# Kernel tuning notes

Measured on AMD Instinct MI355X. Metric: run time of the kernel, lower is better.

The kernel has to match this reference:

```python
import jax, jax.numpy as jnp
import numpy as np

D = 256          # hidden_dim
H = 4            # num_heads
HD = D // H      # head_dim = 64
E = 4            # num_experts (hard-coded in MoE)
TOPK = 2         # top_k (hard-coded)
DFF = 2 * D      # expert ffn width
EPS = 1e-5


def _ln(x, g, b):
    mu = x.mean(-1, keepdims=True)
    var = x.var(-1, keepdims=True)  # biased, matches torch LayerNorm
    return (x - mu) * jax.lax.rsqrt(var + EPS) * g + b


def _ff(x, w1, b1, w2, b2):
    h = jax.nn.gelu(x @ w1 + b1, approximate=False)  # torch nn.GELU default = exact erf
    return h @ w2 + b2


def setup_inputs() -> dict:
    key = jax.random.key(0)
    ks = jax.random.split(key, 24)
    B, S, IN = 4, 2048, 256
    s = 0.02
    inp = {
        'x': jax.random.normal(ks[0], (B, S, IN), jnp.float32),
        'mask': jax.random.randint(ks[1], (B, S), 0, 2).astype(jnp.int32),
        'w_in': jax.random.normal(ks[2], (IN, D), jnp.float32) * s,
        'b_in': jnp.zeros((D,), jnp.float32),
        'g1': jnp.ones((D,), jnp.float32),
        'be1': jnp.zeros((D,), jnp.float32),
        'wq': jax.random.normal(ks[3], (D, D), jnp.float32) * s,
        'bq': jnp.zeros((D,), jnp.float32),
        'wk': jax.random.normal(ks[4], (D, D), jnp.float32) * s,
        'bk': jnp.zeros((D,), jnp.float32),
        'wv': jax.random.normal(ks[5], (D, D), jnp.float32) * s,
        'bv': jnp.zeros((D,), jnp.float32),
        'wo': jax.random.normal(ks[6], (D, D), jnp.float32) * s,
        'bo': jnp.zeros((D,), jnp.float32),
        'g2': jnp.ones((D,), jnp.float32),
        'be2': jnp.zeros((D,), jnp.float32),
        'wg': jax.random.normal(ks[7], (D, E), jnp.float32) * s,
        'bg': jnp.zeros((E,), jnp.float32),
        'ew1': jax.random.normal(ks[8], (E, D, DFF), jnp.float32) * s,
        'eb1': jnp.zeros((E, DFF), jnp.float32),
        'ew2': jax.random.normal(ks[9], (E, DFF, D), jnp.float32) * s,
        'eb2': jnp.zeros((E, D), jnp.float32),
    }
    return inp


def reference(x, mask, w_in, b_in, g1, be1, wq, bq, wk, bk, wv, bv, wo, bo, g2, be2, wg, bg, ew1, eb1, ew2, eb2):
    B, S, _ = x.shape
    x = x @ w_in + b_in
    res = x
    h = _ln(x, g1, be1)
    q = (h @ wq + bq).reshape(B, S, H, HD).transpose(0, 2, 1, 3)  # bhsd
    k = (h @ wk + bk).reshape(B, S, H, HD).transpose(0, 2, 1, 3)
    v = (h @ wv + bv).reshape(B, S, H, HD).transpose(0, 2, 1, 3)
    # RoPE (interleaved pairs, half-concat output, as in source)
    inv_freq = 1.0 / (10000.0 ** (jnp.arange(0, HD, 2, dtype=jnp.float32) / HD))
    ang = jnp.arange(S, dtype=jnp.float32)[:, None] * inv_freq[None, :]  # [S, HD//2]
    sin, cos = jnp.sin(ang), jnp.cos(ang)  # broadcast over (B,H)
    def rot(t):
        ts = t.reshape(B, H, S, HD // 2, 2)
        t0, t1 = ts[..., 0], ts[..., 1]
        return jnp.concatenate([t0 * cos - t1 * sin, t1 * cos + t0 * sin], axis=-1)
    qr, kr = rot(q), rot(k)
    attn = jnp.einsum('bhqd,bhkd->bhqk', qr, kr) * (HD ** -0.5)
    row = mask[:, None, :, None]  # [B,1,S,1] -> masks whole query rows
    attn = jnp.where(row == 0, jnp.float32(-1e4), attn)
    valid = (row * S).astype(jnp.float32)           # [B,1,S,1]
    all_masked = valid == 0
    uniform = jnp.where(row != 0, 1.0 / jnp.maximum(valid, 1.0), 0.0)
    attn = jnp.where(all_masked, uniform, attn)
    attn = jax.nn.softmax(attn, axis=-1)
    out = jnp.einsum('bhqk,bhkd->bhqd', attn, v).transpose(0, 2, 1, 3).reshape(B, S, D)
    out = out @ wo + bo
    x = res + out
    res2 = x
    h2 = _ln(x, g2, be2)
    # MoE (faithful: expert i only applied where top-k slot i picked expert i)
    gp = jax.nn.softmax(h2 @ wg + bg, axis=-1)
    topv, topi = jax.lax.top_k(gp, TOPK)
    moe_out = jnp.zeros_like(h2)
    for i in range(TOPK):
        eo = _ff(h2, ew1[i], eb1[i], ew2[i], eb2[i])
        m = (topi[..., i] == i)[..., None].astype(h2.dtype)
        moe_out = moe_out + m * eo * topv[..., i:i + 1]
    flat = topi.reshape(-1)
    total = sum((flat == i).sum() for i in range(TOPK)).astype(jnp.float32)
    usage = jnp.zeros((E,), jnp.float32) + total
    usage = usage / usage.sum()
    lb = (jnp.std(usage, ddof=1) / usage.mean()) ** 2
    y = res2 + h2  # source discards moe_out / lb (likely a bug); kept live with exact 0* add
    return y + 0.0 * (moe_out.sum() + lb)
```

## Files before the change

kernel.cpp:

```cpp
#include <hip/hip_runtime.h>
#include <cstddef>

#define Bb    4
#define Sq    2048
#define Dd    256
#define Hh    4
#define HDh   64
#define NROWS (Bb*Sq)
#define EPSf  1e-5f

typedef unsigned short u16;
typedef unsigned int   u32;
typedef unsigned long long u64;
typedef __attribute__((ext_vector_type(8))) short  frag_ab;
typedef __attribute__((ext_vector_type(4))) float  frag_cd;

__device__ __forceinline__ u16 f2bf(float f){
    union { float f; u32 u; } v; v.f = f;
    u32 r = v.u + 0x7fffu + ((v.u >> 16) & 1u);
    return (u16)(r >> 16);
}
__device__ __forceinline__ u16 f2bf_trunc(float f){
    union { float f; u32 u; } v; v.f = f;
    return (u16)(v.u >> 16);
}
__device__ __forceinline__ float bf2f(u32 u){
    union { u32 u; float f; } v; v.u = u << 16; return v.f;
}

__global__ __launch_bounds__(256) void k0_prep(
    const float* __restrict__ w_in, const float* __restrict__ wq,
    const float* __restrict__ wk,   const float* __restrict__ wv,
    const float* __restrict__ wo,
    u16* __restrict__ wT, float* __restrict__ tab)
{
    const int bid = blockIdx.x, tid = threadIdx.x;
    if (bid < 80){
        __shared__ float T[64][65];
        const int wsel = bid >> 4, tile = bid & 15;
        const int k0 = (tile >> 2) * 64, n0 = (tile & 3) * 64;
        const float* src = wsel==0 ? w_in : wsel==1 ? wq : wsel==2 ? wk
                         : wsel==3 ? wv : wo;
        #pragma unroll
        for (int i=0;i<16;++i){
            int idx = i*256 + tid, k = idx>>6, n = idx&63;
            T[k][n] = src[(size_t)(k0+k)*Dd + n0 + n];
        }
        __syncthreads();
        u16* dst = wT + (size_t)wsel*Dd*Dd;
        #pragma unroll
        for (int i=0;i<16;++i){
            int idx = i*256 + tid, n = idx>>6, k = idx&63;
            dst[(size_t)(n0+n)*Dd + k0 + k] = f2bf(T[k][n]);
        }
    } else {
        int s = (bid-80)*8 + (tid>>5);
        int p = tid & 31;
        float invf = exp2f(-(float)p * (13.287712379549449f/32.f));
        float sn, cs; sincosf((float)s * invf, &sn, &cs);
        tab[(size_t)s*64 + p]      = cs;
        tab[(size_t)s*64 + 32 + p] = sn;
    }
}

__global__ __launch_bounds__(256) void k1_fused(
    const float* __restrict__ x,  const float* __restrict__ tab,
    const u16* __restrict__ wTin, const u16* __restrict__ wTq,
    const u16* __restrict__ wTk,  const u16* __restrict__ wTv,
    const float* __restrict__ b_in, const float* __restrict__ g1,
    const float* __restrict__ be1,  const float* __restrict__ bq,
    const float* __restrict__ bk,   const float* __restrict__ bv,
    float* __restrict__ x1, u16* __restrict__ qro,
    u16* __restrict__ kro,  u16* __restrict__ vto)
{
    const int tid  = threadIdx.x;
    const int w    = tid >> 6;
    const int lane = tid & 63;
    const int l16  = lane & 15;
    const int quad = lane >> 4;
    const int r0   = blockIdx.x * 16;
    const int b    = r0 >> 11;
    const int s0   = r0 & (Sq-1);
    const int cb   = w * 64;

    __shared__ u16 Xs[16][264];
    __shared__ u16 Hs[16][264];
    __shared__ u16 Os[16][264];
    __shared__ float red[2][16][4];

    #pragma unroll
    for (int i=0;i<4;++i){
        int f = i*256 + tid;
        int row = f>>6, c4 = f&63;
        float4 v4 = *(const float4*)(x + (size_t)(r0+row)*Dd + c4*4);
        u16 pk4[4] = { f2bf(v4.x), f2bf(v4.y), f2bf(v4.z), f2bf(v4.w) };
        *(u64*)&Xs[row][c4*4] = *(u64*)pk4;
    }
    __syncthreads();

    float bin4[4], g4[4], be4[4];
    #pragma unroll
    for (int nt=0;nt<4;++nt){
        int col = cb + nt*16 + l16;
        bin4[nt] = b_in[col]; g4[nt] = g1[col]; be4[nt] = be1[col];
    }

    frag_cd acc[4];
    #pragma unroll
    for (int nt=0;nt<4;++nt) acc[nt] = (frag_cd){bin4[nt],bin4[nt],bin4[nt],bin4[nt]};
    #pragma unroll
    for (int kc=0;kc<8;++kc){
        frag_ab a = *(frag_ab*)&Xs[l16][kc*32 + quad*8];
        #pragma unroll
        for (int nt=0;nt<4;++nt){
            frag_ab bf = *(const frag_ab*)&wTin[(size_t)(cb+nt*16+l16)*Dd + kc*32 + quad*8];
            acc[nt] = __builtin_amdgcn_mfma_f32_16x16x32_bf16(a, bf, acc[nt], 0,0,0);
        }
    }

    #pragma unroll
    for (int r=0;r<4;++r){
        float s=0.f, q=0.f;
        #pragma unroll
        for (int nt=0;nt<4;++nt){
            float v = acc[nt][r];
            x1[(size_t)(r0+quad*4+r)*Dd + cb + nt*16 + l16] = v;
            s += v; q += v*v;
        }
        s += __shfl_xor(s,1); q += __shfl_xor(q,1);
        s += __shfl_xor(s,2); q += __shfl_xor(q,2);
        s += __shfl_xor(s,4); q += __shfl_xor(q,4);
        s += __shfl_xor(s,8); q += __shfl_xor(q,8);
        if (l16==0){ red[0][quad*4+r][w]=s; red[1][quad*4+r][w]=q; }
    }
    __syncthreads();

    #pragma unroll
    for (int r=0;r<4;++r){
        int row = quad*4 + r;
        float mu = (red[0][row][0]+red[0][row][1]+red[0][row][2]+red[0][row][3])*(1.f/Dd);
        float ms = (red[1][row][0]+red[1][row][1]+red[1][row][2]+red[1][row][3])*(1.f/Dd);
        float rstd = rsqrtf(ms - mu*mu + EPSf);
        #pragma unroll
        for (int nt=0;nt<4;++nt){
            float hv = (acc[nt][r]-mu)*rstd*g4[nt] + be4[nt];
            Hs[row][cb + nt*16 + l16] = f2bf(hv);
        }
    }
    __syncthreads();

    const u16*   wps[3] = { wTq, wTk, wTv };
    const float* bps[3] = { bq, bk, bv };
    #pragma unroll
    for (int tt=0; tt<3; ++tt){
        frag_cd a2[4];
        #pragma unroll
        for (int nt=0;nt<4;++nt){
            float bb = bps[tt][cb + nt*16 + l16];
            a2[nt] = (frag_cd){bb,bb,bb,bb};
        }
        #pragma unroll
        for (int kc=0;kc<8;++kc){
            frag_ab a = *(frag_ab*)&Hs[l16][kc*32 + quad*8];
            #pragma unroll
            for (int nt=0;nt<4;++nt){
                frag_ab bf = *(const frag_ab*)&wps[tt][(size_t)(cb+nt*16+l16)*Dd + kc*32 + quad*8];
                a2[nt] = __builtin_amdgcn_mfma_f32_16x16x32_bf16(a, bf, a2[nt], 0,0,0);
            }
        }
        #pragma unroll
        for (int r=0;r<4;++r)
            #pragma unroll
            for (int nt=0;nt<4;++nt)
                Os[quad*4+r][cb + nt*16 + l16] = f2bf(a2[nt][r]);
        __syncthreads();

        if (tt < 2){
            const int row  = tid >> 4;
            const int head = (tid >> 2) & 3;
            const int pq   = tid & 3;
            const int s    = s0 + row;
            const float* tb = tab + (size_t)s*64;
            float4 c0 = *(const float4*)(tb + pq*8);
            float4 c1 = *(const float4*)(tb + pq*8 + 4);
            float4 sn0 = *(const float4*)(tb + 32 + pq*8);
            float4 sn1 = *(const float4*)(tb + 32 + pq*8 + 4);
            const float cA[8] = {c0.x,c0.y,c0.z,c0.w,c1.x,c1.y,c1.z,c1.w};
            const float sA[8] = {sn0.x,sn0.y,sn0.z,sn0.w,sn1.x,sn1.y,sn1.z,sn1.w};
            u16* dst = (tt==0 ? qro : kro) + ((size_t)(b*Hh+head)*Sq + s)*HDh;
            u16 lo[8], hi[8];
            #pragma unroll
            for (int j=0;j<8;++j){
                int p = pq*8 + j;
                u32 pr = *(const u32*)&Os[row][head*64 + 2*p];
                float t0 = bf2f(pr & 0xffffu), t1 = bf2f(pr >> 16);
                lo[j] = f2bf(t0*cA[j] - t1*sA[j]);
                hi[j] = f2bf(t1*cA[j] + t0*sA[j]);
            }
            *(float4*)(dst + pq*8)      = *(float4*)lo;
            *(float4*)(dst + 32 + pq*8) = *(float4*)hi;
        } else {
            const int head = tid >> 6, d = tid & 63;
            u16 pk[16];
            #pragma unroll
            for (int j=0;j<16;++j) pk[j] = Os[j][head*64 + d];
            u16* dst = vto + ((size_t)(b*Hh+head)*HDh + d)*Sq + s0;
            *(float4*)dst     = *(float4*)pk;
            *(float4*)(dst+8) = *(float4*)&pk[8];
        }
        __syncthreads();
    }
}

__global__ __launch_bounds__(256) void k2_attn(
    const u16* __restrict__ qr, const u16* __restrict__ kr,
    const u16* __restrict__ vt, const int* __restrict__ mask,
    float* __restrict__ Opart, float* __restrict__ lpart)
{
    const int tid = threadIdx.x;
    const int w   = tid >> 6;
    const int lane= tid & 63;
    const int l16 = lane & 15;
    const int quad= lane >> 4;
    const int qt  = blockIdx.x;
    const int bh  = blockIdx.y;
    const int ks  = blockIdx.z;
    const int b   = bh >> 2;
    const int q0  = qt * 64;

    __shared__ u16 Qs [64][72];
    __shared__ u16 Ks [64][72];
    __shared__ u16 Vts[64][72];
    __shared__ u16 Ps [4][16][72];

    const u16* qg = qr + ((size_t)bh*Sq + q0)*HDh;
    for (int cc=tid; cc<512; cc+=256){
        int row = cc>>3, part = cc&7;
        *(float4*)&Qs[row][part*8] = *(const float4*)(qg + row*HDh + part*8);
    }
    __syncthreads();

    frag_ab qf0 = *(frag_ab*)&Qs[w*16 + l16][quad*8];
    frag_ab qf1 = *(frag_ab*)&Qs[w*16 + l16][quad*8 + 32];

    float mf2[4];
    #pragma unroll
    for (int r=0;r<4;++r)
        mf2[r] = (mask[(size_t)b*Sq + q0 + w*16 + quad*4 + r] != 0)
               ? 0.125f*1.44269504f : 0.f;

    float lrow[4];
    #pragma unroll
    for (int r=0;r<4;++r) lrow[r] = 0.f;
    frag_cd O[4];
    #pragma unroll
    for (int d=0; d<4; ++d) O[d] = (frag_cd){0.f,0.f,0.f,0.f};

    const u16* kg0 = kr + (size_t)bh*Sq*HDh + (size_t)ks*1024*HDh;
    const u16* vg0 = vt + (size_t)bh*HDh*Sq + (size_t)ks*1024;

    for (int kt=0; kt<16; ++kt){
        __syncthreads();
        const u16* kg = kg0 + (size_t)kt*64*HDh;
        const u16* vg = vg0 + kt*64;
        for (int cc=tid; cc<512; cc+=256){
            int row = cc>>3, part = cc&7;
            *(float4*)&Ks[row][part*8]  = *(const float4*)(kg + row*HDh  + part*8);
            *(float4*)&Vts[row][part*8] = *(const float4*)(vg + (size_t)row*Sq + part*8);
        }
        __syncthreads();

        frag_cd sc[4];
        #pragma unroll
        for (int t=0;t<4;++t){
            frag_ab kf0 = *(frag_ab*)&Ks[t*16 + l16][quad*8];
            frag_ab kf1 = *(frag_ab*)&Ks[t*16 + l16][quad*8 + 32];
            frag_cd z = (frag_cd){0.f,0.f,0.f,0.f};
            z = __builtin_amdgcn_mfma_f32_16x16x32_bf16(qf0, kf0, z, 0,0,0);
            z = __builtin_amdgcn_mfma_f32_16x16x32_bf16(qf1, kf1, z, 0,0,0);
            sc[t] = z;
        }

        #pragma unroll
        for (int t=0;t<4;++t)
            #pragma unroll
            for (int r=0;r<4;++r){
                float p = exp2f(sc[t][r]*mf2[r]);
                lrow[r] += p;
                Ps[w][quad*4+r][t*16 + l16] = f2bf_trunc(p);
            }

        frag_ab pf0 = *(frag_ab*)&Ps[w][l16][quad*8];
        frag_ab pf1 = *(frag_ab*)&Ps[w][l16][quad*8 + 32];

        #pragma unroll
        for (int d=0; d<4; ++d){
            frag_ab vf0 = *(frag_ab*)&Vts[d*16 + l16][quad*8];
            frag_ab vf1 = *(frag_ab*)&Vts[d*16 + l16][quad*8 + 32];
            O[d] = __builtin_amdgcn_mfma_f32_16x16x32_bf16(pf0, vf0, O[d], 0,0,0);
            O[d] = __builtin_amdgcn_mfma_f32_16x16x32_bf16(pf1, vf1, O[d], 0,0,0);
        }
    }

    float* Ob = Opart + (((size_t)ks*16 + bh)*Sq)*HDh;
    #pragma unroll
    for (int r=0;r<4;++r){
        size_t ro = (size_t)(q0 + w*16 + quad*4 + r)*HDh + l16;
        #pragma unroll
        for (int d=0; d<4; ++d)
            Ob[ro + d*16] = O[d][r];
        float s = lrow[r];
        s += __shfl_xor(s,1);
        s += __shfl_xor(s,2);
        s += __shfl_xor(s,4);
        s += __shfl_xor(s,8);
        if (l16 == 0)
            lpart[((size_t)ks*16 + bh)*Sq + q0 + w*16 + quad*4 + r] = s;
    }
}

__global__ __launch_bounds__(256) void k3_gemm_ln(
    const float* __restrict__ Opart, const float* __restrict__ lpart,
    const u16* __restrict__ wTo,
    const float* __restrict__ bo, const float* __restrict__ x1,
    const float* __restrict__ g2, const float* __restrict__ be2,
    float* __restrict__ out)
{
    const int tid  = threadIdx.x;
    const int w    = tid >> 6;
    const int lane = tid & 63;
    const int l16  = lane & 15;
    const int quad = lane >> 4;
    const int r0   = blockIdx.x * 16;
    const int b    = r0 >> 11;
    const int s0   = r0 & (Sq-1);
    const int cb   = w * 64;

    __shared__ u16 Ats[16][264];
    __shared__ float red[2][16][4];
    __shared__ float linv[4][16];

    if (tid < 64){
        int h = tid >> 4, r = tid & 15;
        size_t li = ((size_t)(b*Hh + h))*Sq + s0 + r;
        linv[h][r] = 1.f / (lpart[li] + lpart[(size_t)16*Sq + li]);
    }
    __syncthreads();

    const size_t SPLIT = (size_t)16*Sq*HDh;
    #pragma unroll
    for (int i=0;i<4;++i){
        int idx = i*256 + tid;
        int h = idx >> 8, rem = idx & 255, row = rem >> 4, c = rem & 15;
        size_t base = (((size_t)(b*Hh + h))*Sq + s0 + row)*HDh + c*4;
        float4 o0 = *(const float4*)(Opart + base);
        float4 o1 = *(const float4*)(Opart + SPLIT + base);
        float li = linv[h][row];
        u16 pk[4] = { f2bf((o0.x+o1.x)*li), f2bf((o0.y+o1.y)*li),
                      f2bf((o0.z+o1.z)*li), f2bf((o0.w+o1.w)*li) };
        *(u64*)&Ats[row][h*64 + c*4] = *(u64*)pk;
    }
    __syncthreads();

    float g4[4], be4[4];
    frag_cd acc[4];
    #pragma unroll
    for (int nt=0;nt<4;++nt){
        int col = cb + nt*16 + l16;
        float bb = bo[col];
        acc[nt] = (frag_cd){bb,bb,bb,bb};
        g4[nt] = g2[col]; be4[nt] = be2[col];
    }
    #pragma unroll
    for (int kc=0;kc<8;++kc){
        frag_ab a = *(frag_ab*)&Ats[l16][kc*32 + quad*8];
        #pragma unroll
        for (int nt=0;nt<4;++nt){
            frag_ab bf = *(const frag_ab*)&wTo[(size_t)(cb+nt*16+l16)*Dd + kc*32 + quad*8];
            acc[nt] = __builtin_amdgcn_mfma_f32_16x16x32_bf16(a, bf, acc[nt], 0,0,0);
        }
    }

    #pragma unroll
    for (int r=0;r<4;++r){
        float s=0.f, q=0.f;
        #pragma unroll
        for (int nt=0;nt<4;++nt){
            float v = acc[nt][r] + x1[(size_t)(r0+quad*4+r)*Dd + cb + nt*16 + l16];
            acc[nt][r] = v;
            s += v; q += v*v;
        }
        s += __shfl_xor(s,1); q += __shfl_xor(q,1);
        s += __shfl_xor(s,2); q += __shfl_xor(q,2);
        s += __shfl_xor(s,4); q += __shfl_xor(q,4);
        s += __shfl_xor(s,8); q += __shfl_xor(q,8);
        if (l16==0){ red[0][quad*4+r][w]=s; red[1][quad*4+r][w]=q; }
    }
    __syncthreads();

    #pragma unroll
    for (int r=0;r<4;++r){
        int row = quad*4 + r;
        float mu = (red[0][row][0]+red[0][row][1]+red[0][row][2]+red[0][row][3])*(1.f/Dd);
        float ms = (red[1][row][0]+red[1][row][1]+red[1][row][2]+red[1][row][3])*(1.f/Dd);
        float rstd = rsqrtf(ms - mu*mu + EPSf);
        #pragma unroll
        for (int nt=0;nt<4;++nt){
            float v = acc[nt][r];
            float h2 = (v-mu)*rstd*g4[nt] + be4[nt];
            out[(size_t)(r0+row)*Dd + cb + nt*16 + l16] = v + h2;
        }
    }
}

extern "C" void kernel_launch(void* const* d_in, const int* in_sizes, int n_in,
                              void* d_out, int out_size, void* d_ws, size_t ws_size,
                              hipStream_t stream)
{
    const float* x    = (const float*)d_in[0];
    const int*   mask = (const int*)  d_in[1];
    const float* w_in = (const float*)d_in[2];
    const float* b_in = (const float*)d_in[3];
    const float* g1   = (const float*)d_in[4];
    const float* be1  = (const float*)d_in[5];
    const float* wq   = (const float*)d_in[6];
    const float* bq   = (const float*)d_in[7];
    const float* wk   = (const float*)d_in[8];
    const float* bk   = (const float*)d_in[9];
    const float* wv   = (const float*)d_in[10];
    const float* bv   = (const float*)d_in[11];
    const float* wo   = (const float*)d_in[12];
    const float* bo   = (const float*)d_in[13];
    const float* g2   = (const float*)d_in[14];
    const float* be2  = (const float*)d_in[15];

    float* out = (float*)d_out;
    char*  wsb = (char*)d_ws;

    float* x1    = (float*)(wsb);
    float* tab   = (float*)(wsb + ( 8u<<20));
    u16*   qro   = (u16*)(wsb + (12u<<20));
    u16*   kro   = (u16*)(wsb + (16u<<20));
    u16*   vto   = (u16*)(wsb + (20u<<20));
    float* Opart = (float*)(wsb + (24u<<20));
    float* lpart = (float*)(wsb + (40u<<20));
    u16*   wT    = (u16*)(wsb + (40u<<20) + (512u<<10));

    k0_prep<<<336, 256, 0, stream>>>(w_in, wq, wk, wv, wo, wT, tab);
    k1_fused<<<NROWS/16, 256, 0, stream>>>(
        x, tab, wT, wT + Dd*Dd, wT + 2*Dd*Dd, wT + 3*Dd*Dd,
        b_in, g1, be1, bq, bk, bv, x1, qro, kro, vto);
    k2_attn<<<dim3(Sq/64, Bb*Hh, 2), 256, 0, stream>>>(qro, kro, vto, mask, Opart, lpart);
    k3_gemm_ln<<<NROWS/16, 256, 0, stream>>>(Opart, lpart, wT + 4*Dd*Dd,
                                             bo, x1, g2, be2, out);
}
```

Measured before the change: 189.8 us.

## Swap MFMA operands for row-contiguous vector stores and store attention partials in bf16

The MFMA A/B operands are swapped in every GEMM and in the attention kernel, so each lane holds four consecutive columns of one row. Epilogues (x1, Hs, Os, out, P tiles, attention output) can then use float4/u64 vector stores, and row reductions shrink to two cross-quad shuffles. The split-K attention partial outputs are now stored as bf16 instead of fp32, which halves that intermediate traffic but adds a rounding step before the combine. Biases and LN parameters are loaded as float4.

Result: no change. 193.3 us (+1.9%).

```diff
diff --git a/kernel.cpp b/kernel.cpp
--- a/kernel.cpp
+++ b/kernel.cpp
@@ -82,6 +82,7 @@
     const int b    = r0 >> 11;
     const int s0   = r0 & (Sq-1);
     const int cb   = w * 64;
+    const int c4   = cb + quad*4;
 
     __shared__ u16 Xs[16][264];
     __shared__ u16 Hs[16][264];
@@ -91,60 +92,55 @@
     #pragma unroll
     for (int i=0;i<4;++i){
         int f = i*256 + tid;
-        int row = f>>6, c4 = f&63;
-        float4 v4 = *(const float4*)(x + (size_t)(r0+row)*Dd + c4*4);
+        int row = f>>6, cc = f&63;
+        float4 v4 = *(const float4*)(x + (size_t)(r0+row)*Dd + cc*4);
         u16 pk4[4] = { f2bf(v4.x), f2bf(v4.y), f2bf(v4.z), f2bf(v4.w) };
-        *(u64*)&Xs[row][c4*4] = *(u64*)pk4;
-    }
-    __syncthreads();
-
-    float bin4[4], g4[4], be4[4];
+        *(u64*)&Xs[row][cc*4] = *(u64*)pk4;
+    }
+    __syncthreads();
+
+    frag_cd acc[4];
     #pragma unroll
     for (int nt=0;nt<4;++nt){
-        int col = cb + nt*16 + l16;
-        bin4[nt] = b_in[col]; g4[nt] = g1[col]; be4[nt] = be1[col];
-    }
-
-    frag_cd acc[4];
-    #pragma unroll
-    for (int nt=0;nt<4;++nt) acc[nt] = (frag_cd){bin4[nt],bin4[nt],bin4[nt],bin4[nt]};
+        float4 b4 = *(const float4*)&b_in[c4 + nt*16];
+        acc[nt] = (frag_cd){b4.x, b4.y, b4.z, b4.w};
+    }
     #pragma unroll
     for (int kc=0;kc<8;++kc){
-        frag_ab a = *(frag_ab*)&Xs[l16][kc*32 + quad*8];
-        #pragma unroll
-        for (int nt=0;nt<4;++nt){
-            frag_ab bf = *(const frag_ab*)&wTin[(size_t)(cb+nt*16+l16)*Dd + kc*32 + quad*8];
-            acc[nt] = __builtin_amdgcn_mfma_f32_16x16x32_bf16(a, bf, acc[nt], 0,0,0);
-        }
-    }
-
-    #pragma unroll
-    for (int r=0;r<4;++r){
-        float s=0.f, q=0.f;
-        #pragma unroll
-        for (int nt=0;nt<4;++nt){
-            float v = acc[nt][r];
-            x1[(size_t)(r0+quad*4+r)*Dd + cb + nt*16 + l16] = v;
-            s += v; q += v*v;
-        }
-        s += __shfl_xor(s,1); q += __shfl_xor(q,1);
-        s += __shfl_xor(s,2); q += __shfl_xor(q,2);
-        s += __shfl_xor(s,4); q += __shfl_xor(q,4);
-        s += __shfl_xor(s,8); q += __shfl_xor(q,8);
-        if (l16==0){ red[0][quad*4+r][w]=s; red[1][quad*4+r][w]=q; }
-    }
-    __syncthreads();
-
-    #pragma unroll
-    for (int r=0;r<4;++r){
-        int row = quad*4 + r;
-        float mu = (red[0][row][0]+red[0][row][1]+red[0][row][2]+red[0][row][3])*(1.f/Dd);
-        float ms = (red[1][row][0]+red[1][row][1]+red[1][row][2]+red[1][row][3])*(1.f/Dd);
+        frag_ab xa = *(frag_ab*)&Xs[l16][kc*32 + quad*8];
+        #pragma unroll
+        for (int nt=0;nt<4;++nt){
+            frag_ab wf = *(const frag_ab*)&wTin[(size_t)(cb+nt*16+l16)*Dd + kc*32 + quad*8];
+            acc[nt] = __builtin_amdgcn_mfma_f32_16x16x32_bf16(wf, xa, acc[nt], 0,0,0);
+        }
+    }
+
+    float s=0.f, q=0.f;
+    #pragma unroll
+    for (int nt=0;nt<4;++nt){
+        float4 v4 = make_float4(acc[nt][0], acc[nt][1], acc[nt][2], acc[nt][3]);
+        *(float4*)&x1[(size_t)(r0+l16)*Dd + c4 + nt*16] = v4;
+        s += v4.x+v4.y+v4.z+v4.w;
+        q += v4.x*v4.x + v4.y*v4.y + v4.z*v4.z + v4.w*v4.w;
+    }
+    s += __shfl_xor(s,16); q += __shfl_xor(q,16);
+    s += __shfl_xor(s,32); q += __shfl_xor(q,32);
+    if (lane < 16){ red[0][l16][w]=s; red[1][l16][w]=q; }
+    __syncthreads();
+
+    {
+        float mu = (red[0][l16][0]+red[0][l16][1]+red[0][l16][2]+red[0][l16][3])*(1.f/Dd);
+        float ms = (red[1][l16][0]+red[1][l16][1]+red[1][l16][2]+red[1][l16][3])*(1.f/Dd);
         float rstd = rsqrtf(ms - mu*mu + EPSf);
         #pragma unroll
         for (int nt=0;nt<4;++nt){
-            float hv = (acc[nt][r]-mu)*rstd*g4[nt] + be4[nt];
-            Hs[row][cb + nt*16 + l16] = f2bf(hv);
+            float4 g4 = *(const float4*)&g1[c4 + nt*16];
+            float4 e4 = *(const float4*)&be1[c4 + nt*16];
+            u16 pk4[4] = { f2bf((acc[nt][0]-mu)*rstd*g4.x + e4.x),
+                           f2bf((acc[nt][1]-mu)*rstd*g4.y + e4.y),
+                           f2bf((acc[nt][2]-mu)*rstd*g4.z + e4.z),
+                           f2bf((acc[nt][3]-mu)*rstd*g4.w + e4.w) };
+            *(u64*)&Hs[l16][c4 + nt*16] = *(u64*)pk4;
         }
     }
     __syncthreads();
@@ -156,38 +152,39 @@
         frag_cd a2[4];
         #pragma unroll
         for (int nt=0;nt<4;++nt){
-            float bb = bps[tt][cb + nt*16 + l16];
-            a2[nt] = (frag_cd){bb,bb,bb,bb};
+            float4 b4 = *(const float4*)&bps[tt][c4 + nt*16];
+            a2[nt] = (frag_cd){b4.x, b4.y, b4.z, b4.w};
         }
         #pragma unroll
         for (int kc=0;kc<8;++kc){
-            frag_ab a = *(frag_ab*)&Hs[l16][kc*32 + quad*8];
+            frag_ab ha = *(frag_ab*)&Hs[l16][kc*32 + quad*8];
             #pragma unroll
             for (int nt=0;nt<4;++nt){
-                frag_ab bf = *(const frag_ab*)&wps[tt][(size_t)(cb+nt*16+l16)*Dd + kc*32 + quad*8];
-                a2[nt] = __builtin_amdgcn_mfma_f32_16x16x32_bf16(a, bf, a2[nt], 0,0,0);
+                frag_ab wf = *(const frag_ab*)&wps[tt][(size_t)(cb+nt*16+l16)*Dd + kc*32 + quad*8];
+                a2[nt] = __builtin_amdgcn_mfma_f32_16x16x32_bf16(wf, ha, a2[nt], 0,0,0);
             }
         }
         #pragma unroll
-        for (int r=0;r<4;++r)
-            #pragma unroll
-            for (int nt=0;nt<4;++nt)
-                Os[quad*4+r][cb + nt*16 + l16] = f2bf(a2[nt][r]);
+        for (int nt=0;nt<4;++nt){
+            u16 pk4[4] = { f2bf(a2[nt][0]), f2bf(a2[nt][1]),
+                           f2bf(a2[nt][2]), f2bf(a2[nt][3]) };
+            *(u64*)&Os[l16][c4 + nt*16] = *(u64*)pk4;
+        }
         __syncthreads();
 
         if (tt < 2){
             const int row  = tid >> 4;
             const int head = (tid >> 2) & 3;
             const int pq   = tid & 3;
-            const int s    = s0 + row;
-            const float* tb = tab + (size_t)s*64;
+            const int sidx = s0 + row;
+            const float* tb = tab + (size_t)sidx*64;
             float4 c0 = *(const float4*)(tb + pq*8);
             float4 c1 = *(const float4*)(tb + pq*8 + 4);
             float4 sn0 = *(const float4*)(tb + 32 + pq*8);
             float4 sn1 = *(const float4*)(tb + 32 + pq*8 + 4);
             const float cA[8] = {c0.x,c0.y,c0.z,c0.w,c1.x,c1.y,c1.z,c1.w};
             const float sA[8] = {sn0.x,sn0.y,sn0.z,sn0.w,sn1.x,sn1.y,sn1.z,sn1.w};
-            u16* dst = (tt==0 ? qro : kro) + ((size_t)(b*Hh+head)*Sq + s)*HDh;
+            u16* dst = (tt==0 ? qro : kro) + ((size_t)(b*Hh+head)*Sq + sidx)*HDh;
             u16 lo[8], hi[8];
             #pragma unroll
             for (int j=0;j<8;++j){
@@ -215,7 +212,7 @@
 __global__ __launch_bounds__(256) void k2_attn(
     const u16* __restrict__ qr, const u16* __restrict__ kr,
     const u16* __restrict__ vt, const int* __restrict__ mask,
-    float* __restrict__ Opart, float* __restrict__ lpart)
+    u16* __restrict__ Opart, float* __restrict__ lpart)
 {
     const int tid = threadIdx.x;
     const int w   = tid >> 6;
@@ -243,15 +240,10 @@
     frag_ab qf0 = *(frag_ab*)&Qs[w*16 + l16][quad*8];
     frag_ab qf1 = *(frag_ab*)&Qs[w*16 + l16][quad*8 + 32];
 
-    float mf2[4];
-    #pragma unroll
-    for (int r=0;r<4;++r)
-        mf2[r] = (mask[(size_t)b*Sq + q0 + w*16 + quad*4 + r] != 0)
-               ? 0.125f*1.44269504f : 0.f;
-
-    float lrow[4];
-    #pragma unroll
-    for (int r=0;r<4;++r) lrow[r] = 0.f;
+    const float mf2 = (mask[(size_t)b*Sq + q0 + w*16 + l16] != 0)
+                    ? 0.125f*1.44269504f : 0.f;
+
+    float lsum = 0.f;
     frag_cd O[4];
     #pragma unroll
     for (int d=0; d<4; ++d) O[d] = (frag_cd){0.f,0.f,0.f,0.f};
@@ -276,19 +268,22 @@
             frag_ab kf0 = *(frag_ab*)&Ks[t*16 + l16][quad*8];
             frag_ab kf1 = *(frag_ab*)&Ks[t*16 + l16][quad*8 + 32];
             frag_cd z = (frag_cd){0.f,0.f,0.f,0.f};
-            z = __builtin_amdgcn_mfma_f32_16x16x32_bf16(qf0, kf0, z, 0,0,0);
-            z = __builtin_amdgcn_mfma_f32_16x16x32_bf16(qf1, kf1, z, 0,0,0);
+            z = __builtin_amdgcn_mfma_f32_16x16x32_bf16(kf0, qf0, z, 0,0,0);
+            z = __builtin_amdgcn_mfma_f32_16x16x32_bf16(kf1, qf1, z, 0,0,0);
             sc[t] = z;
         }
 
         #pragma unroll
-        for (int t=0;t<4;++t)
-            #pragma unroll
-            for (int r=0;r<4;++r){
-                float p = exp2f(sc[t][r]*mf2[r]);
-                lrow[r] += p;
-                Ps[w][quad*4+r][t*16 + l16] = f2bf_trunc(p);
-            }
+        for (int t=0;t<4;++t){
+            float p0 = exp2f(sc[t][0]*mf2);
+            float p1 = exp2f(sc[t][1]*mf2);
+            float p2 = exp2f(sc[t][2]*mf2);
+            float p3 = exp2f(sc[t][3]*mf2);
+            lsum += p0+p1+p2+p3;
+            u16 pk4[4] = { f2bf_trunc(p0), f2bf_trunc(p1),
+                           f2bf_trunc(p2), f2bf_trunc(p3) };
+            *(u64*)&Ps[w][l16][t*16 + quad*4] = *(u64*)pk4;
+        }
 
         frag_ab pf0 = *(frag_ab*)&Ps[w][l16][quad*8];
         frag_ab pf1 = *(frag_ab*)&Ps[w][l16][quad*8 + 32];
@@ -297,30 +292,26 @@
         for (int d=0; d<4; ++d){
             frag_ab vf0 = *(frag_ab*)&Vts[d*16 + l16][quad*8];
             frag_ab vf1 = *(frag_ab*)&Vts[d*16 + l16][quad*8 + 32];
-            O[d] = __builtin_amdgcn_mfma_f32_16x16x32_bf16(pf0, vf0, O[d], 0,0,0);
-            O[d] = __builtin_amdgcn_mfma_f32_16x16x32_bf16(pf1, vf1, O[d], 0,0,0);
-        }
-    }
-
-    float* Ob = Opart + (((size_t)ks*16 + bh)*Sq)*HDh;
-    #pragma unroll
-    for (int r=0;r<4;++r){
-        size_t ro = (size_t)(q0 + w*16 + quad*4 + r)*HDh + l16;
-        #pragma unroll
-        for (int d=0; d<4; ++d)
-            Ob[ro + d*16] = O[d][r];
-        float s = lrow[r];
-        s += __shfl_xor(s,1);
-        s += __shfl_xor(s,2);
-        s += __shfl_xor(s,4);
-        s += __shfl_xor(s,8);
-        if (l16 == 0)
-            lpart[((size_t)ks*16 + bh)*Sq + q0 + w*16 + quad*4 + r] = s;
-    }
+            O[d] = __builtin_amdgcn_mfma_f32_16x16x32_bf16(vf0, pf0, O[d], 0,0,0);
+            O[d] = __builtin_amdgcn_mfma_f32_16x16x32_bf16(vf1, pf1, O[d], 0,0,0);
+        }
+    }
+
+    u16* Ob = Opart + (((size_t)ks*16 + bh)*Sq + q0 + w*16 + l16)*HDh;
+    #pragma unroll
+    for (int dt=0; dt<4; ++dt){
+        u16 pk4[4] = { f2bf(O[dt][0]), f2bf(O[dt][1]),
+                       f2bf(O[dt][2]), f2bf(O[dt][3]) };
+        *(u64*)(Ob + dt*16 + quad*4) = *(u64*)pk4;
+    }
+    lsum += __shfl_xor(lsum,16);
+    lsum += __shfl_xor(lsum,32);
+    if (lane < 16)
+        lpart[((size_t)ks*16 + bh)*Sq + q0 + w*16 + l16] = lsum;
 }
 
 __global__ __launch_bounds__(256) void k3_gemm_ln(
-    const float* __restrict__ Opart, const float* __restrict__ lpart,
+    const u16* __restrict__ Opart, const float* __restrict__ lpart,
     const u16* __restrict__ wTo,
     const float* __restrict__ bo, const float* __restrict__ x1,
     const float* __restrict__ g2, const float* __restrict__ be2,
@@ -335,6 +326,7 @@
     const int b    = r0 >> 11;
     const int s0   = r0 & (Sq-1);
     const int cb   = w * 64;
+    const int c4   = cb + quad*4;
 
     __shared__ u16 Ats[16][264];
     __shared__ float red[2][16][4];
@@ -353,62 +345,65 @@
         int idx = i*256 + tid;
         int h = idx >> 8, rem = idx & 255, row = rem >> 4, c = rem & 15;
         size_t base = (((size_t)(b*Hh + h))*Sq + s0 + row)*HDh + c*4;
-        float4 o0 = *(const float4*)(Opart + base);
-        float4 o1 = *(const float4*)(Opart + SPLIT + base);
+        u64 p0 = *(const u64*)(Opart + base);
+        u64 p1 = *(const u64*)(Opart + SPLIT + base);
         float li = linv[h][row];
-        u16 pk[4] = { f2bf((o0.x+o1.x)*li), f2bf((o0.y+o1.y)*li),
-                      f2bf((o0.z+o1.z)*li), f2bf((o0.w+o1.w)*li) };
+        u16 pk[4];
+        #pragma unroll
+        for (int j=0;j<4;++j){
+            float v0 = bf2f((u32)((p0 >> (16*j)) & 0xffffu));
+            float v1 = bf2f((u32)((p1 >> (16*j)) & 0xffffu));
+            pk[j] = f2bf((v0+v1)*li);
+        }
         *(u64*)&Ats[row][h*64 + c*4] = *(u64*)pk;
     }
     __syncthreads();
 
-    float g4[4], be4[4];
     frag_cd acc[4];
     #pragma unroll
     for (int nt=0;nt<4;++nt){
-        int col = cb + nt*16 + l16;
-        float bb = bo[col];
-        acc[nt] = (frag_cd){bb,bb,bb,bb};
-        g4[nt] = g2[col]; be4[nt] = be2[col];
+        float4 b4 = *(const float4*)&bo[c4 + nt*16];
+        acc[nt] = (frag_cd){b4.x, b4.y, b4.z, b4.w};
     }
     #pragma unroll
     for (int kc=0;kc<8;++kc){
-        frag_ab a = *(frag_ab*)&Ats[l16][kc*32 + quad*8];
-        #pragma unroll
-        for (int nt=0;nt<4;++nt){
-            frag_ab bf = *(const frag_ab*)&wTo[(size_t)(cb+nt*16+l16)*Dd + kc*32 + quad*8];
-            acc[nt] = __builtin_amdgcn_mfma_f32_16x16x32_bf16(a, bf, acc[nt], 0,0,0);
-        }
-    }
-
-    #pragma unroll
-    for (int r=0;r<4;++r){
-        float s=0.f, q=0.f;
-        #pragma unroll
-        for (int nt=0;nt<4;++nt){
-            float v = acc[nt][r] + x1[(size_t)(r0+quad*4+r)*Dd + cb + nt*16 + l16];
-            acc[nt][r] = v;
-            s += v; q += v*v;
-        }
-        s += __shfl_xor(s,1); q += __shfl_xor(q,1);
-        s += __shfl_xor(s,2); q += __shfl_xor(q,2);
-        s += __shfl_xor(s,4); q += __shfl_xor(q,4);
-        s += __shfl_xor(s,8); q += __shfl_xor(q,8);
-        if (l16==0){ red[0][quad*4+r][w]=s; red[1][quad*4+r][w]=q; }
-    }
-    __syncthreads();
-
-    #pragma unroll
-    for (int r=0;r<4;++r){
-        int row = quad*4 + r;
-        float mu = (red[0][row][0]+red[0][row][1]+red[0][row][2]+red[0][row][3])*(1.f/Dd);
-        float ms = (red[1][row][0]+red[1][row][1]+red[1][row][2]+red[1][row][3])*(1.f/Dd);
+        frag_ab aa = *(frag_ab*)&Ats[l16][kc*32 + quad*8];
+        #pragma unroll
+        for (int nt=0;nt<4;++nt){
+            frag_ab wf = *(const frag_ab*)&wTo[(size_t)(cb+nt*16+l16)*Dd + kc*32 + quad*8];
+            acc[nt] = __builtin_amdgcn_mfma_f32_16x16x32_bf16(wf, aa, acc[nt], 0,0,0);
+        }
+    }
+
+    float s=0.f, q=0.f;
+    #pragma unroll
+    for (int nt=0;nt<4;++nt){
+        float4 r4 = *(const float4*)&x1[(size_t)(r0+l16)*Dd + c4 + nt*16];
+        acc[nt][0] += r4.x; acc[nt][1] += r4.y;
+        acc[nt][2] += r4.z; acc[nt][3] += r4.w;
+        s += acc[nt][0]+acc[nt][1]+acc[nt][2]+acc[nt][3];
+        q += acc[nt][0]*acc[nt][0] + acc[nt][1]*acc[nt][1]
+           + acc[nt][2]*acc[nt][2] + acc[nt][3]*acc[nt][3];
+    }
+    s += __shfl_xor(s,16); q += __shfl_xor(q,16);
+    s += __shfl_xor(s,32); q += __shfl_xor(q,32);
+    if (lane < 16){ red[0][l16][w]=s; red[1][l16][w]=q; }
+    __syncthreads();
+
+    {
+        float mu = (red[0][l16][0]+red[0][l16][1]+red[0][l16][2]+red[0][l16][3])*(1.f/Dd);
+        float ms = (red[1][l16][0]+red[1][l16][1]+red[1][l16][2]+red[1][l16][3])*(1.f/Dd);
         float rstd = rsqrtf(ms - mu*mu + EPSf);
         #pragma unroll
         for (int nt=0;nt<4;++nt){
-            float v = acc[nt][r];
-            float h2 = (v-mu)*rstd*g4[nt] + be4[nt];
-            out[(size_t)(r0+row)*Dd + cb + nt*16 + l16] = v + h2;
+            float4 g4 = *(const float4*)&g2[c4 + nt*16];
+            float4 e4 = *(const float4*)&be2[c4 + nt*16];
+            float4 o4;
+            o4.x = acc[nt][0] + (acc[nt][0]-mu)*rstd*g4.x + e4.x;
+            o4.y = acc[nt][1] + (acc[nt][1]-mu)*rstd*g4.y + e4.y;
+            o4.z = acc[nt][2] + (acc[nt][2]-mu)*rstd*g4.z + e4.z;
+            o4.w = acc[nt][3] + (acc[nt][3]-mu)*rstd*g4.w + e4.w;
+            *(float4*)&out[(size_t)(r0+l16)*Dd + c4 + nt*16] = o4;
         }
     }
 }
@@ -442,9 +437,9 @@
     u16*   qro   = (u16*)(wsb + (12u<<20));
     u16*   kro   = (u16*)(wsb + (16u<<20));
     u16*   vto   = (u16*)(wsb + (20u<<20));
-    float* Opart = (float*)(wsb + (24u<<20));
-    float* lpart = (float*)(wsb + (40u<<20));
-    u16*   wT    = (u16*)(wsb + (40u<<20) + (512u<<10));
+    u16*   Opart = (u16*)(wsb + (24u<<20));
+    float* lpart = (float*)(wsb + (32u<<20));
+    u16*   wT    = (u16*)(wsb + (33u<<20));
 
     k0_prep<<<336, 256, 0, stream>>>(w_in, wq, wk, wv, wo, wT, tab);
     k1_fused<<<NROWS/16, 256, 0, stream>>>(
```
